# Kernel optimization log

Measured on AMD Instinct MI355X. Metric: run time of the kernel, lower is better.

## Reference

```python
import jax, jax.numpy as jnp
import numpy as np

D_MODEL = 1024
HEADS = 16
HEAD_DIM = D_MODEL // HEADS
EPS = 1e-6


def feature_map(x):
    # F.elu(x) + 1
    return jax.nn.elu(x) + 1.0


def setup_inputs() -> dict:
    key = jax.random.key(0)
    ks = jax.random.split(key, 9)
    B, N, D = 4, 4096, D_MODEL
    s = 1.0 / np.sqrt(D)
    return {
        "x": jax.random.normal(ks[0], (B, N, D), dtype=jnp.float32),
        "Wq": jax.random.normal(ks[1], (D, D), dtype=jnp.float32) * s,
        "bq": jnp.zeros((D,), dtype=jnp.float32),
        "Wk": jax.random.normal(ks[2], (D, D), dtype=jnp.float32) * s,
        "bk": jnp.zeros((D,), dtype=jnp.float32),
        "Wv": jax.random.normal(ks[3], (D, D), dtype=jnp.float32) * s,
        "bv": jnp.zeros((D,), dtype=jnp.float32),
        "Wo": jax.random.normal(ks[4], (D, D), dtype=jnp.float32) * s,
        "bo": jnp.zeros((D,), dtype=jnp.float32),
    }


def reference(x, Wq, bq, Wk, bk, Wv, bv, Wo, bo):
    B, N, D = x.shape
    H, hd = HEADS, HEAD_DIM
    # torch Linear: y = x @ W.T + b
    q = feature_map((x @ Wq.T + bq).reshape(B, N, H, hd))
    k = feature_map((x @ Wk.T + bk).reshape(B, N, H, hd))
    v = (x @ Wv.T + bv).reshape(B, N, H, hd)
    k_sum = k.sum(axis=1)                                   # (B, H, hd)
    D_inv = 1.0 / (jnp.einsum('bnhd,bhd->bnh', q, k_sum) + EPS)
    context = jnp.einsum('bnhd,bnhv->bhdv', k, v)            # (B, H, hd, hd)
    out = jnp.einsum('bnhd,bhdv->bnhv', q, context) * D_inv[..., None]
    out = out.reshape(B, N, D)
    return out @ Wo.T + bo
```

## Files before the change

kernel.cpp:

```cpp
#include <hip/hip_runtime.h>
#include <hip/hip_bf16.h>

typedef __attribute__((ext_vector_type(8))) short bf16x8;
typedef __attribute__((ext_vector_type(4))) float f32x4;

__device__ __forceinline__ float b2f(unsigned short u) {
  union { unsigned int i; float f; } x; x.i = ((unsigned int)u) << 16; return x.f;
}
__device__ __forceinline__ unsigned short f2b(float f) {
  union { __hip_bfloat16 h; unsigned short u; } x; x.h = __float2bfloat16(f); return x.u;
}
__device__ __forceinline__ f32x4 mfma16(bf16x8 a, bf16x8 b, f32x4 c) {
  return __builtin_amdgcn_mfma_f32_16x16x32_bf16(a, b, c, 0, 0, 0);
}
__device__ __forceinline__ void gl16(const void* g, void* l) {
  __builtin_amdgcn_global_load_lds(
      (const __attribute__((address_space(1))) unsigned int*)g,
      (__attribute__((address_space(3))) unsigned int*)l, 16, 0, 0);
}

__global__ __launch_bounds__(256) void cast_k(const float* __restrict__ src,
                                              unsigned short* __restrict__ dst, int n4) {
  int i = blockIdx.x * 256 + threadIdx.x;
  if (i >= n4) return;
  float4 v = ((const float4*)src)[i];
  ushort4 o;
  o.x = f2b(v.x); o.y = f2b(v.y); o.z = f2b(v.z); o.w = f2b(v.w);
  ((ushort4*)dst)[i] = o;
}

#define BARX() asm volatile("s_barrier" ::: "memory")
#define LGKM0() asm volatile("s_waitcnt lgkmcnt(0)" ::: "memory")
#define WAITV4() asm volatile("s_waitcnt vmcnt(4)" ::: "memory")
#define WAITV0() asm volatile("s_waitcnt vmcnt(0)" ::: "memory")
#define P1() __builtin_amdgcn_s_setprio(1)
#define P0() __builtin_amdgcn_s_setprio(0)

#define STAGE_A(BUF, G, TAU) do { \
  gl16(gA_0 + (size_t)(G) * 65536 + (TAU) * 64, sAB + (BUF) * 32768 + (G) * 16384 + u0 * 16); \
  gl16(gA_1 + (size_t)(G) * 65536 + (TAU) * 64, sAB + (BUF) * 32768 + (G) * 16384 + u1 * 16); } while (0)
#define STAGE_B(BUF, G, TAU) do { \
  gl16(gB_0 + (size_t)(G) * 32768 + (TAU) * 64, sAB + 65536 + (BUF) * 32768 + (G) * 16384 + u0 * 16); \
  gl16(gB_1 + (size_t)(G) * 32768 + (TAU) * 64, sAB + 65536 + (BUF) * 32768 + (G) * 16384 + u1 * 16); } while (0)

#define LOAD_A(BUF, MH) do { \
  _Pragma("unroll") for (int mi = 0; mi < 4; ++mi) { \
    const char* p_ = (const char*)sAB + (BUF) * 32768 + (MH) * 16384 + aRd + mi * 2048; \
    af[mi][0] = *(const bf16x8*)(p_ + sr0); \
    af[mi][1] = *(const bf16x8*)(p_ + sr1); } } while (0)
#define LOAD_B(BUF, NH, DST) do { \
  _Pragma("unroll") for (int ni = 0; ni < 2; ++ni) { \
    const char* p_ = (const char*)sAB + 65536 + (BUF) * 32768 + (NH) * 16384 + bRd + ni * 2048; \
    DST[ni][0] = *(const bf16x8*)(p_ + sr0); \
    DST[ni][1] = *(const bf16x8*)(p_ + sr1); } } while (0)

#define QUAD(MH, NH, BF) do { \
  _Pragma("unroll") for (int mi = 0; mi < 4; ++mi) \
    _Pragma("unroll") for (int ni = 0; ni < 2; ++ni) { \
      acc[(MH) * 4 + mi][(NH) * 2 + ni] = mfma16(af[mi][0], BF[ni][0], acc[(MH) * 4 + mi][(NH) * 2 + ni]); \
      acc[(MH) * 4 + mi][(NH) * 2 + ni] = mfma16(af[mi][1], BF[ni][1], acc[(MH) * 4 + mi][(NH) * 2 + ni]); } } while (0)

template<int MODE>
__global__ __launch_bounds__(512, 2) void gemm256(
    const unsigned short* __restrict__ A,
    const unsigned short* __restrict__ W0, const unsigned short* __restrict__ W1,
    const unsigned short* __restrict__ W2,
    const float* __restrict__ bias0, const float* __restrict__ bias1, const float* __restrict__ bias2,
    float* __restrict__ outF,
    unsigned short* __restrict__ o0, unsigned short* __restrict__ o1, unsigned short* __restrict__ o2,
    int tiles_m, float* __restrict__ ksum)
{
  __shared__ char sAB[131072];
  int bid = blockIdx.x;
  int nwg = gridDim.x;
  int cpx = nwg >> 3;
  int sbid = (bid & 7) * cpx + (bid >> 3);
  int tm = sbid % tiles_m, tn = sbid / tiles_m;
  int m0 = tm * 256, n0 = tn * 256;

  const unsigned short* W = W0; const float* bias = bias0; unsigned short* outB = o0;
  int sel = 0;
  if (MODE == 1) {
    sel = n0 >> 10;
    if (sel == 1) { W = W1; bias = bias1; outB = o1; }
    else if (sel == 2) { W = W2; bias = bias2; outB = o2; }
  }
  int nloc0 = (MODE == 1) ? (n0 & 1023) : n0;

  int t = threadIdx.x, w = t >> 6, l = t & 63;
  int wm = w >> 2, wn = w & 3;

  int u0 = t, u1 = t + 512;
  int lr0 = u0 >> 3, lr1 = u1 >> 3;
  int sl0 = (u0 & 7) ^ (lr0 & 7), sl1 = (u1 & 7) ^ (lr1 & 7);
  int rA0 = ((lr0 >> 6) << 7) + (lr0 & 63), rA1 = ((lr1 >> 6) << 7) + (lr1 & 63);
  int rB0 = ((lr0 >> 5) << 6) + (lr0 & 31), rB1 = ((lr1 >> 5) << 6) + (lr1 & 31);
  const unsigned short* gA_0 = A + (size_t)(m0 + rA0) * 1024 + sl0 * 8;
  const unsigned short* gA_1 = A + (size_t)(m0 + rA1) * 1024 + sl1 * 8;
  const unsigned short* gB_0 = W + (size_t)(nloc0 + rB0) * 1024 + sl0 * 8;
  const unsigned short* gB_1 = W + (size_t)(nloc0 + rB1) * 1024 + sl1 * 8;

  int aRd = (wm * 64 + (l & 15)) * 128;
  int bRd = (wn * 32 + (l & 15)) * 128;
  int sr0 = (((l >> 4) + 0) ^ (l & 7)) * 16;
  int sr1 = (((l >> 4) + 4) ^ (l & 7)) * 16;

  f32x4 acc[8][4];
  f32x4 zero = {0.f, 0.f, 0.f, 0.f};
#pragma unroll
  for (int i = 0; i < 8; ++i)
#pragma unroll
    for (int jx = 0; jx < 4; ++jx) acc[i][jx] = zero;
  bf16x8 af[4][2], bf0[2][2], bf1[2][2];

  STAGE_A(0, 0, 0); STAGE_B(0, 0, 0); STAGE_A(0, 1, 0); STAGE_B(0, 1, 0);
  STAGE_A(1, 0, 1); STAGE_B(1, 0, 1);
  WAITV4();
  BARX();

  for (int j = 0; j < 8; ++j) {
    int t1 = 2 * j + 1;
    int t2 = (j < 7) ? (2 * j + 2) : 14;
    int t3 = (j < 7) ? (2 * j + 3) : 15;
    LOAD_A(0, 0); LOAD_B(0, 0, bf0);
    STAGE_A(1, 1, t1);
    BARX(); LGKM0(); P1(); QUAD(0, 0, bf0); P0(); BARX();
    LOAD_B(0, 1, bf1);
    STAGE_B(1, 1, t1);
    BARX(); LGKM0(); P1(); QUAD(0, 1, bf1); P0(); BARX();
    LOAD_A(0, 1);
    STAGE_A(0, 0, t2);
    BARX(); LGKM0(); P1(); QUAD(1, 0, bf0); P0(); BARX();
    STAGE_B(0, 0, t2);
    BARX(); LGKM0(); P1(); QUAD(1, 1, bf1); P0(); WAITV4(); BARX();
    LOAD_A(1, 0); LOAD_B(1, 0, bf0);
    STAGE_A(0, 1, t2);
    BARX(); LGKM0(); P1(); QUAD(0, 0, bf0); P0(); BARX();
    LOAD_B(1, 1, bf1);
    STAGE_B(0, 1, t2);
    BARX(); LGKM0(); P1(); QUAD(0, 1, bf1); P0(); BARX();
    LOAD_A(1, 1);
    STAGE_A(1, 0, t3);
    BARX(); LGKM0(); P1(); QUAD(1, 0, bf0); P0(); BARX();
    STAGE_B(1, 0, t3);
    BARX(); LGKM0(); P1(); QUAD(1, 1, bf1); P0(); WAITV4(); BARX();
  }
  WAITV0();

  if (MODE == 1 && sel >= 1) {
    int b_idx = m0 >> 12;
    int nloc_h = nloc0 >> 6;
#pragma unroll
    for (int mq = 0; mq < 8; ++mq) {
      int r_base = wm * 128 + (mq >> 2) * 64 + (mq & 3) * 16 + ((l >> 4) << 2);
#pragma unroll
      for (int nq = 0; nq < 4; ++nq) {
        int c_loc = wn * 64 + (nq >> 1) * 32 + (nq & 1) * 16 + (l & 15);
        float bb = bias[nloc0 + c_loc];
        float v0 = acc[mq][nq][0] + bb, v1 = acc[mq][nq][1] + bb;
        float v2 = acc[mq][nq][2] + bb, v3 = acc[mq][nq][3] + bb;
        if (sel == 1) {
          v0 = (v0 > 0.0f) ? (v0 + 1.0f) : __expf(v0);
          v1 = (v1 > 0.0f) ? (v1 + 1.0f) : __expf(v1);
          v2 = (v2 > 0.0f) ? (v2 + 1.0f) : __expf(v2);
          v3 = (v3 > 0.0f) ? (v3 + 1.0f) : __expf(v3);
        }
        unsigned long long pk =
            (unsigned long long)(f2b(v0) | ((unsigned int)f2b(v1) << 16)) |
            ((unsigned long long)(f2b(v2) | ((unsigned int)f2b(v3) << 16)) << 32);
        int byte = c_loc * 512 + ((r_base * 2) ^ ((c_loc & 7) << 4));
        *(unsigned long long*)(sAB + byte) = pk;
      }
    }
    __syncthreads();
#pragma unroll
    for (int qq = 0; qq < 16; ++qq) {
      int c_loc = qq * 16 + w * 2 + (l >> 5);
      int n_off = (l & 31) * 8;
      int d = c_loc & 63;
      int bh = b_idx * 16 + nloc_h + (c_loc >> 6);
      int byte = c_loc * 512 + ((n_off * 2) ^ ((c_loc & 7) << 4));
      bf16x8 ch = *(const bf16x8*)(sAB + byte);
      *(bf16x8*)(outB + (size_t)(bh * 64 + d) * 4096 + (m0 & 4095) + n_off) = ch;
      if (sel == 1) {
        float s = 0.f;
#pragma unroll
        for (int jj = 0; jj < 8; ++jj) s += b2f((unsigned short)ch[jj]);
        s += __shfl_xor(s, 1);
        s += __shfl_xor(s, 2);
        s += __shfl_xor(s, 4);
        s += __shfl_xor(s, 8);
        s += __shfl_xor(s, 16);
        if ((l & 31) == 0) atomicAdd(ksum + bh * 64 + d, s);
      }
    }
  } else {
#pragma unroll
    for (int mq = 0; mq < 8; ++mq) {
      int grow = m0 + wm * 128 + (mq >> 2) * 64 + (mq & 3) * 16 + ((l >> 4) << 2);
#pragma unroll
      for (int nq = 0; nq < 4; ++nq) {
        int gcol = n0 + wn * 64 + (nq >> 1) * 32 + (nq & 1) * 16 + (l & 15);
        if (MODE == 0) {
          float bb = bias[gcol];
#pragma unroll
          for (int r = 0; r < 4; ++r)
            outF[(size_t)(grow + r) * 1024 + gcol] = acc[mq][nq][r] + bb;
        } else {
          int c = gcol & 1023;
          float bb = bias[c];
#pragma unroll
          for (int r = 0; r < 4; ++r) {
            float v = acc[mq][nq][r] + bb;
            v = (v > 0.0f) ? (v + 1.0f) : __expf(v);
            outB[(size_t)(grow + r) * 1024 + c] = f2b(v);
          }
        }
      }
    }
  }
}

__global__ __launch_bounds__(256) void ctx_gemm(
    const unsigned short* __restrict__ vT,
    const unsigned short* __restrict__ kT,
    float* __restrict__ ctxT)
{
  __shared__ float red[4][64 * 65];
  int bid = blockIdx.x;
  int bh = bid >> 3, ch = bid & 7;
  int t = threadIdx.x, wv = t >> 6, l = t & 63;
  int noff = ch * 512 + wv * 128 + ((l >> 4) << 3);
  const unsigned short* aB = vT + ((size_t)bh * 64 + (l & 15)) * 4096 + noff;
  const unsigned short* bB = kT + ((size_t)bh * 64 + (l & 15)) * 4096 + noff;
  f32x4 acc[4][4];
  f32x4 zero = {0.f, 0.f, 0.f, 0.f};
#pragma unroll
  for (int i = 0; i < 4; ++i)
#pragma unroll
    for (int j = 0; j < 4; ++j) acc[i][j] = zero;
  for (int ks = 0; ks < 4; ++ks) {
    bf16x8 av[4], bv[4];
#pragma unroll
    for (int mi = 0; mi < 4; ++mi) av[mi] = *(const bf16x8*)(aB + (size_t)mi * 16 * 4096 + ks * 32);
#pragma unroll
    for (int ni = 0; ni < 4; ++ni) bv[ni] = *(const bf16x8*)(bB + (size_t)ni * 16 * 4096 + ks * 32);
#pragma unroll
    for (int mi = 0; mi < 4; ++mi)
#pragma unroll
      for (int ni = 0; ni < 4; ++ni)
        acc[mi][ni] = mfma16(av[mi], bv[ni], acc[mi][ni]);
  }
#pragma unroll
  for (int mi = 0; mi < 4; ++mi)
#pragma unroll
    for (int ni = 0; ni < 4; ++ni)
#pragma unroll
      for (int r = 0; r < 4; ++r) {
        int e = mi * 16 + ((l >> 4) << 2) + r;
        int d = ni * 16 + (l & 15);
        red[wv][e * 65 + d] = acc[mi][ni][r];
      }
  __syncthreads();
  for (int o = t; o < 4096; o += 256) {
    int idx = (o >> 6) * 65 + (o & 63);
    float s = red[0][idx] + red[1][idx] + red[2][idx] + red[3][idx];
    atomicAdd(ctxT + (size_t)bh * 4096 + o, s);
  }
}

__global__ __launch_bounds__(256) void att_gemm(
    unsigned short* __restrict__ q,
    const float* __restrict__ ctxT,
    const float* __restrict__ ksum)
{
  int bid = blockIdx.x;
  int bh = bid & 63, mt = bid >> 6;
  int b = bh >> 4, h = bh & 15;
  int t = threadIdx.x, w = t >> 6, l = t & 63;
  int m0 = mt * 256 + w * 64;

  bf16x8 bfr[2][4];
  const float* cb = ctxT + (size_t)bh * 4096;
#pragma unroll
  for (int ks = 0; ks < 2; ++ks)
#pragma unroll
    for (int ni = 0; ni < 4; ++ni) {
      const float* p = cb + (ni * 16 + (l & 15)) * 64 + ks * 32 + ((l >> 4) << 3);
#pragma unroll
      for (int j = 0; j < 8; ++j) bfr[ks][ni][j] = (short)f2b(p[j]);
    }

  const float* kp = ksum + bh * 64 + ((l >> 4) << 3);
  float kp0[8], kp1[8];
#pragma unroll
  for (int j = 0; j < 8; ++j) { kp0[j] = kp[j]; kp1[j] = kp[j + 32]; }

  f32x4 acc[4][4];
  f32x4 zero = {0.f, 0.f, 0.f, 0.f};
#pragma unroll
  for (int i = 0; i < 4; ++i)
#pragma unroll
    for (int j = 0; j < 4; ++j) acc[i][j] = zero;
  float dvv[4];

  size_t rowbase = (size_t)(b * 4096 + m0 + (l & 15)) * 1024 + h * 64 + ((l >> 4) << 3);
#pragma unroll
  for (int mi = 0; mi < 4; ++mi) {
    bf16x8 av0 = *(const bf16x8*)(q + rowbase + (size_t)mi * 16 * 1024);
    bf16x8 av1 = *(const bf16x8*)(q + rowbase + (size_t)mi * 16 * 1024 + 32);
    float s = 0.f;
#pragma unroll
    for (int j = 0; j < 8; ++j) {
      s += b2f((unsigned short)av0[j]) * kp0[j];
      s += b2f((unsigned short)av1[j]) * kp1[j];
    }
    s += __shfl_xor(s, 16);
    s += __shfl_xor(s, 32);
    dvv[mi] = 1.0f / (s + 1e-6f);
#pragma unroll
    for (int ni = 0; ni < 4; ++ni) {
      acc[mi][ni] = mfma16(av0, bfr[0][ni], acc[mi][ni]);
      acc[mi][ni] = mfma16(av1, bfr[1][ni], acc[mi][ni]);
    }
  }

#pragma unroll
  for (int mi = 0; mi < 4; ++mi) {
    float sc[4];
#pragma unroll
    for (int r = 0; r < 4; ++r) sc[r] = __shfl(dvv[mi], ((l >> 4) << 2) + r);
#pragma unroll
    for (int ni = 0; ni < 4; ++ni) {
      int e = ni * 16 + (l & 15);
#pragma unroll
      for (int r = 0; r < 4; ++r) {
        int npos = m0 + mi * 16 + ((l >> 4) << 2) + r;
        q[(size_t)(b * 4096 + npos) * 1024 + h * 64 + e] = f2b(acc[mi][ni][r] * sc[r]);
      }
    }
  }
}

extern "C" void kernel_launch(void* const* d_in, const int* in_sizes, int n_in,
                              void* d_out, int out_size, void* d_ws, size_t ws_size,
                              hipStream_t stream)
{
  const float* x  = (const float*)d_in[0];
  const float* bq = (const float*)d_in[2];
  const float* bk = (const float*)d_in[4];
  const float* bv = (const float*)d_in[6];
  const float* bo = (const float*)d_in[8];
  const float* Wq = (const float*)d_in[1];
  const float* Wk = (const float*)d_in[3];
  const float* Wv = (const float*)d_in[5];
  const float* Wo = (const float*)d_in[7];
  float* out = (float*)d_out;

  char* ws = (char*)d_ws;
  const size_t SB = (size_t)16384 * 1024 * 2;
  const size_t NEED = 4 * SB + 4 * (1u << 21) + 2 * (1u << 20) + (1u << 14);
  if (ws_size < NEED) return;

  unsigned short* xb  = (unsigned short*)(ws);
  unsigned short* qb  = (unsigned short*)(ws + SB);
  unsigned short* kTb = (unsigned short*)(ws + 2 * SB);
  unsigned short* vTb = (unsigned short*)(ws + 3 * SB);
  unsigned short* wqb = (unsigned short*)(ws + 4 * SB);
  unsigned short* wkb = (unsigned short*)(ws + 4 * SB + (1u << 21));
  unsigned short* wvb = (unsigned short*)(ws + 4 * SB + (2u << 21));
  unsigned short* wob = (unsigned short*)(ws + 4 * SB + (3u << 21));
  float* ctxT = (float*)(ws + 4 * SB + (4u << 21));
  float* ksum = (float*)(ws + 4 * SB + (4u << 21) + (2u << 20));

  hipMemsetAsync(ctxT, 0, 64 * 64 * 64 * 4, stream);
  hipMemsetAsync(ksum, 0, 64 * 64 * 4, stream);

  cast_k<<<16384, 256, 0, stream>>>(x, xb, 16777216 / 4);
  cast_k<<<1024, 256, 0, stream>>>(Wq, wqb, 1048576 / 4);
  cast_k<<<1024, 256, 0, stream>>>(Wk, wkb, 1048576 / 4);
  cast_k<<<1024, 256, 0, stream>>>(Wv, wvb, 1048576 / 4);
  cast_k<<<1024, 256, 0, stream>>>(Wo, wob, 1048576 / 4);

  gemm256<1><<<768, 512, 0, stream>>>(xb, wqb, wkb, wvb, bq, bk, bv,
                                      nullptr, qb, kTb, vTb, 64, ksum);

  ctx_gemm<<<512, 256, 0, stream>>>(vTb, kTb, ctxT);

  att_gemm<<<1024, 256, 0, stream>>>(qb, ctxT, ksum);

  gemm256<0><<<256, 512, 0, stream>>>(qb, wob, nullptr, nullptr, bo, nullptr, nullptr,
                                      out, nullptr, nullptr, nullptr, 64, nullptr);
}
```

Before: 250.9 us.

## Fold context matrix into output projection weights per batch

The per-head context matrix is pre-multiplied into Wo, giving a per-batch weight M_b. The attention GEMM is replaced by a lightweight D_inv row scaling of q, and the final GEMM then uses M_b directly. The four weight casts are merged into one launch, and the GEMM tile order is swapped to N-major with a changed tile count parameter. This removes the att_gemm pass over q, at the cost of an extra bf16 rounding of ctx·Wo and per-batch weight reads in the final GEMM.

```diff
diff --git a/kernel.cpp b/kernel.cpp
--- a/kernel.cpp
+++ b/kernel.cpp
@@ -27,6 +27,21 @@
   ushort4 o;
   o.x = f2b(v.x); o.y = f2b(v.y); o.z = f2b(v.z); o.w = f2b(v.w);
   ((ushort4*)dst)[i] = o;
+}
+
+__global__ __launch_bounds__(256) void castw_k(
+    const float* __restrict__ s0, const float* __restrict__ s1,
+    const float* __restrict__ s2, const float* __restrict__ s3,
+    unsigned short* __restrict__ d0, unsigned short* __restrict__ d1,
+    unsigned short* __restrict__ d2, unsigned short* __restrict__ d3) {
+  int seg = blockIdx.x >> 10;
+  int i = (blockIdx.x & 1023) * 256 + threadIdx.x;
+  const float* s = (seg == 0) ? s0 : (seg == 1) ? s1 : (seg == 2) ? s2 : s3;
+  unsigned short* d = (seg == 0) ? d0 : (seg == 1) ? d1 : (seg == 2) ? d2 : d3;
+  float4 v = ((const float4*)s)[i];
+  ushort4 o;
+  o.x = f2b(v.x); o.y = f2b(v.y); o.z = f2b(v.z); o.w = f2b(v.w);
+  ((ushort4*)d)[i] = o;
 }
 
 #define BARX() asm volatile("s_barrier" ::: "memory")
@@ -68,14 +83,14 @@
     const float* __restrict__ bias0, const float* __restrict__ bias1, const float* __restrict__ bias2,
     float* __restrict__ outF,
     unsigned short* __restrict__ o0, unsigned short* __restrict__ o1, unsigned short* __restrict__ o2,
-    int tiles_m, float* __restrict__ ksum)
+    int tiles_n, float* __restrict__ ksum)
 {
   __shared__ char sAB[131072];
   int bid = blockIdx.x;
   int nwg = gridDim.x;
   int cpx = nwg >> 3;
   int sbid = (bid & 7) * cpx + (bid >> 3);
-  int tm = sbid % tiles_m, tn = sbid / tiles_m;
+  int tn = sbid % tiles_n, tm = sbid / tiles_n;
   int m0 = tm * 256, n0 = tn * 256;
 
   const unsigned short* W = W0; const float* bias = bias0; unsigned short* outB = o0;
@@ -84,6 +99,8 @@
     sel = n0 >> 10;
     if (sel == 1) { W = W1; bias = bias1; outB = o1; }
     else if (sel == 2) { W = W2; bias = bias2; outB = o2; }
+  } else {
+    W = W0 + ((size_t)(m0 >> 12) << 20);
   }
   int nloc0 = (MODE == 1) ? (n0 & 1023) : n0;
 
@@ -222,8 +239,8 @@
 }
 
 __global__ __launch_bounds__(256) void ctx_gemm(
+    const unsigned short* __restrict__ kT,
     const unsigned short* __restrict__ vT,
-    const unsigned short* __restrict__ kT,
     float* __restrict__ ctxT)
 {
   __shared__ float red[4][64 * 65];
@@ -231,8 +248,8 @@
   int bh = bid >> 3, ch = bid & 7;
   int t = threadIdx.x, wv = t >> 6, l = t & 63;
   int noff = ch * 512 + wv * 128 + ((l >> 4) << 3);
-  const unsigned short* aB = vT + ((size_t)bh * 64 + (l & 15)) * 4096 + noff;
-  const unsigned short* bB = kT + ((size_t)bh * 64 + (l & 15)) * 4096 + noff;
+  const unsigned short* aB = kT + ((size_t)bh * 64 + (l & 15)) * 4096 + noff;
+  const unsigned short* bB = vT + ((size_t)bh * 64 + (l & 15)) * 4096 + noff;
   f32x4 acc[4][4];
   f32x4 zero = {0.f, 0.f, 0.f, 0.f};
 #pragma unroll
@@ -257,9 +274,9 @@
     for (int ni = 0; ni < 4; ++ni)
 #pragma unroll
       for (int r = 0; r < 4; ++r) {
-        int e = mi * 16 + ((l >> 4) << 2) + r;
-        int d = ni * 16 + (l & 15);
-        red[wv][e * 65 + d] = acc[mi][ni][r];
+        int dd = mi * 16 + ((l >> 4) << 2) + r;
+        int vv = ni * 16 + (l & 15);
+        red[wv][dd * 65 + vv] = acc[mi][ni][r];
       }
   __syncthreads();
   for (int o = t; o < 4096; o += 256) {
@@ -269,77 +286,88 @@
   }
 }
 
-__global__ __launch_bounds__(256) void att_gemm(
+__global__ __launch_bounds__(1024) void ctxwo_k(
+    const float* __restrict__ ctxT,
+    const unsigned short* __restrict__ wo,
+    unsigned short* __restrict__ M)
+{
+  int bh = blockIdx.x;
+  int b = bh >> 4, h = bh & 15;
+  int t = threadIdx.x, wv = t >> 6, l = t & 63;
+  int j0 = wv * 64;
+
+  bf16x8 af[4][2], bf[4][2];
+#pragma unroll
+  for (int mi = 0; mi < 4; ++mi)
+#pragma unroll
+    for (int ks = 0; ks < 2; ++ks)
+      af[mi][ks] = *(const bf16x8*)(wo + (size_t)(j0 + mi * 16 + (l & 15)) * 1024 +
+                                    h * 64 + ((l >> 4) << 3) + ks * 32);
+#pragma unroll
+  for (int ni = 0; ni < 4; ++ni)
+#pragma unroll
+    for (int ks = 0; ks < 2; ++ks) {
+      const float* p = ctxT + (size_t)bh * 4096 + (ni * 16 + (l & 15)) * 64 +
+                       ((l >> 4) << 3) + ks * 32;
+#pragma unroll
+      for (int jj = 0; jj < 8; ++jj) bf[ni][ks][jj] = (short)f2b(p[jj]);
+    }
+
+  f32x4 acc[4][4];
+  f32x4 zero = {0.f, 0.f, 0.f, 0.f};
+#pragma unroll
+  for (int i = 0; i < 4; ++i)
+#pragma unroll
+    for (int j = 0; j < 4; ++j) acc[i][j] = zero;
+#pragma unroll
+  for (int mi = 0; mi < 4; ++mi)
+#pragma unroll
+    for (int ni = 0; ni < 4; ++ni) {
+      acc[mi][ni] = mfma16(af[mi][0], bf[ni][0], acc[mi][ni]);
+      acc[mi][ni] = mfma16(af[mi][1], bf[ni][1], acc[mi][ni]);
+    }
+
+  unsigned short* Mb = M + ((size_t)b << 20);
+#pragma unroll
+  for (int mi = 0; mi < 4; ++mi)
+#pragma unroll
+    for (int ni = 0; ni < 4; ++ni)
+#pragma unroll
+      for (int r = 0; r < 4; ++r) {
+        int j = j0 + mi * 16 + ((l >> 4) << 2) + r;
+        int d = ni * 16 + (l & 15);
+        Mb[(size_t)j * 1024 + h * 64 + d] = f2b(acc[mi][ni][r]);
+      }
+}
+
+__global__ __launch_bounds__(256) void dinvq_k(
     unsigned short* __restrict__ q,
-    const float* __restrict__ ctxT,
     const float* __restrict__ ksum)
 {
-  int bid = blockIdx.x;
-  int bh = bid & 63, mt = bid >> 6;
-  int b = bh >> 4, h = bh & 15;
-  int t = threadIdx.x, w = t >> 6, l = t & 63;
-  int m0 = mt * 256 + w * 64;
-
-  bf16x8 bfr[2][4];
-  const float* cb = ctxT + (size_t)bh * 4096;
-#pragma unroll
-  for (int ks = 0; ks < 2; ++ks)
-#pragma unroll
-    for (int ni = 0; ni < 4; ++ni) {
-      const float* p = cb + (ni * 16 + (l & 15)) * 64 + ks * 32 + ((l >> 4) << 3);
-#pragma unroll
-      for (int j = 0; j < 8; ++j) bfr[ks][ni][j] = (short)f2b(p[j]);
-    }
-
-  const float* kp = ksum + bh * 64 + ((l >> 4) << 3);
-  float kp0[8], kp1[8];
-#pragma unroll
-  for (int j = 0; j < 8; ++j) { kp0[j] = kp[j]; kp1[j] = kp[j + 32]; }
-
-  f32x4 acc[4][4];
-  f32x4 zero = {0.f, 0.f, 0.f, 0.f};
-#pragma unroll
-  for (int i = 0; i < 4; ++i)
-#pragma unroll
-    for (int j = 0; j < 4; ++j) acc[i][j] = zero;
-  float dvv[4];
-
-  size_t rowbase = (size_t)(b * 4096 + m0 + (l & 15)) * 1024 + h * 64 + ((l >> 4) << 3);
-#pragma unroll
-  for (int mi = 0; mi < 4; ++mi) {
-    bf16x8 av0 = *(const bf16x8*)(q + rowbase + (size_t)mi * 16 * 1024);
-    bf16x8 av1 = *(const bf16x8*)(q + rowbase + (size_t)mi * 16 * 1024 + 32);
-    float s = 0.f;
-#pragma unroll
-    for (int j = 0; j < 8; ++j) {
-      s += b2f((unsigned short)av0[j]) * kp0[j];
-      s += b2f((unsigned short)av1[j]) * kp1[j];
-    }
-    s += __shfl_xor(s, 16);
-    s += __shfl_xor(s, 32);
-    dvv[mi] = 1.0f / (s + 1e-6f);
-#pragma unroll
-    for (int ni = 0; ni < 4; ++ni) {
-      acc[mi][ni] = mfma16(av0, bfr[0][ni], acc[mi][ni]);
-      acc[mi][ni] = mfma16(av1, bfr[1][ni], acc[mi][ni]);
-    }
-  }
-
-#pragma unroll
-  for (int mi = 0; mi < 4; ++mi) {
-    float sc[4];
-#pragma unroll
-    for (int r = 0; r < 4; ++r) sc[r] = __shfl(dvv[mi], ((l >> 4) << 2) + r);
-#pragma unroll
-    for (int ni = 0; ni < 4; ++ni) {
-      int e = ni * 16 + (l & 15);
-#pragma unroll
-      for (int r = 0; r < 4; ++r) {
-        int npos = m0 + mi * 16 + ((l >> 4) << 2) + r;
-        q[(size_t)(b * 4096 + npos) * 1024 + h * 64 + e] = f2b(acc[mi][ni][r] * sc[r]);
-      }
-    }
-  }
+  int t = threadIdx.x, wv = t >> 6, l = t & 63;
+  int n = blockIdx.x * 4 + wv;
+  int b = n >> 12;
+  int h = l >> 2;
+  unsigned short* qp = q + (size_t)n * 1024 + l * 16;
+  const float* kp = ksum + (b * 16 + h) * 64 + (l & 3) * 16;
+  bf16x8 v0 = *(const bf16x8*)qp;
+  bf16x8 v1 = *(const bf16x8*)(qp + 8);
+  float s = 0.f;
+#pragma unroll
+  for (int j = 0; j < 8; ++j) {
+    s += b2f((unsigned short)v0[j]) * kp[j];
+    s += b2f((unsigned short)v1[j]) * kp[8 + j];
+  }
+  s += __shfl_xor(s, 1);
+  s += __shfl_xor(s, 2);
+  float di = 1.0f / (s + 1e-6f);
+#pragma unroll
+  for (int j = 0; j < 8; ++j) {
+    v0[j] = (short)f2b(b2f((unsigned short)v0[j]) * di);
+    v1[j] = (short)f2b(b2f((unsigned short)v1[j]) * di);
+  }
+  *(bf16x8*)qp = v0;
+  *(bf16x8*)(qp + 8) = v1;
 }
 
 extern "C" void kernel_launch(void* const* d_in, const int* in_sizes, int n_in,
@@ -372,23 +400,23 @@
   unsigned short* wob = (unsigned short*)(ws + 4 * SB + (3u << 21));
   float* ctxT = (float*)(ws + 4 * SB + (4u << 21));
   float* ksum = (float*)(ws + 4 * SB + (4u << 21) + (2u << 20));
+  unsigned short* Mbuf = xb;
 
   hipMemsetAsync(ctxT, 0, 64 * 64 * 64 * 4, stream);
   hipMemsetAsync(ksum, 0, 64 * 64 * 4, stream);
 
   cast_k<<<16384, 256, 0, stream>>>(x, xb, 16777216 / 4);
-  cast_k<<<1024, 256, 0, stream>>>(Wq, wqb, 1048576 / 4);
-  cast_k<<<1024, 256, 0, stream>>>(Wk, wkb, 1048576 / 4);
-  cast_k<<<1024, 256, 0, stream>>>(Wv, wvb, 1048576 / 4);
-  cast_k<<<1024, 256, 0, stream>>>(Wo, wob, 1048576 / 4);
+  castw_k<<<4096, 256, 0, stream>>>(Wq, Wk, Wv, Wo, wqb, wkb, wvb, wob);
 
   gemm256<1><<<768, 512, 0, stream>>>(xb, wqb, wkb, wvb, bq, bk, bv,
-                                      nullptr, qb, kTb, vTb, 64, ksum);
-
-  ctx_gemm<<<512, 256, 0, stream>>>(vTb, kTb, ctxT);
-
-  att_gemm<<<1024, 256, 0, stream>>>(qb, ctxT, ksum);
-
-  gemm256<0><<<256, 512, 0, stream>>>(qb, wob, nullptr, nullptr, bo, nullptr, nullptr,
-                                      out, nullptr, nullptr, nullptr, 64, nullptr);
-}
+                                      nullptr, qb, kTb, vTb, 12, ksum);
+
+  ctx_gemm<<<512, 256, 0, stream>>>(kTb, vTb, ctxT);
+
+  ctxwo_k<<<64, 1024, 0, stream>>>(ctxT, wob, Mbuf);
+
+  dinvq_k<<<4096, 256, 0, stream>>>(qb, ksum);
+
+  gemm256<0><<<256, 512, 0, stream>>>(qb, Mbuf, nullptr, nullptr, bo, nullptr, nullptr,
+                                      out, nullptr, nullptr, nullptr, 4, nullptr);
+}
```

New measurement: 229.8 us. 1.09x faster.
